# Performance work log

Measured on AMD Instinct MI355X. Metric: run time of the kernel, lower is better.

Reference implementation:

```python
import jax, jax.numpy as jnp
import numpy as np

THRESH = 0.7  # TWN-style threshold factor: delta = 0.7 * mean|W|


def ternarize(W):
    """Quantize latent float weights to alpha * {-1, 0, +1} (per-tensor scale)."""
    absW = jnp.abs(W)
    delta = THRESH * jnp.mean(absW)
    mask = (absW > delta).astype(W.dtype)
    n = jnp.maximum(jnp.sum(mask), 1.0)
    alpha = jnp.sum(absW * mask) / n
    return alpha * jnp.sign(W) * mask


def setup_inputs() -> dict:
    key = jax.random.key(0)
    k_x, k_w1, k_b1, k_w2, k_b2 = jax.random.split(key, 5)
    B = 65536
    x = jax.random.normal(k_x, (B, 784), dtype=jnp.float32)
    # latent float weights (torch Linear layout: [out, in]), kaiming-ish scale
    W1 = jax.random.normal(k_w1, (64, 784), dtype=jnp.float32) * (1.0 / np.sqrt(784))
    b1 = jax.random.normal(k_b1, (64,), dtype=jnp.float32) * 0.01
    W2 = jax.random.normal(k_w2, (10, 64), dtype=jnp.float32) * (1.0 / np.sqrt(64))
    b2 = jax.random.normal(k_b2, (10,), dtype=jnp.float32) * 0.01
    return {"x": x, "W1": W1, "b1": b1, "W2": W2, "b2": b2}


def reference(x, W1, b1, W2, b2):
    x = x.reshape(-1, 784)
    Wq1 = ternarize(W1)  # [64, 784]
    Wq2 = ternarize(W2)  # [10, 64]
    h = jax.nn.relu(x @ Wq1.T + b1)   # [B, 64]
    out = h @ Wq2.T + b2              # [B, 10]
    return out
```

## Files before the change

### kernel.cpp

```cpp
#include <hip/hip_runtime.h>
#include <hip/hip_bf16.h>


typedef __attribute__((ext_vector_type(4))) float f32x4;
typedef __attribute__((ext_vector_type(8))) short s16x8;
typedef __attribute__((ext_vector_type(4))) short s16x4;

#define K1 784
#define K1_PAD 800
#define NHID 64
#define NOUT 10

static __device__ __forceinline__ unsigned short f2bf_rne(float f) {
    unsigned int u = __builtin_bit_cast(unsigned int, f);
    unsigned int r = u + 0x7FFFu + ((u >> 16) & 1u);
    return (unsigned short)(r >> 16);
}

static __device__ double block_sum256(double v, double* red) {
    #pragma unroll
    for (int off = 32; off > 0; off >>= 1) v += __shfl_down(v, off, 64);
    const int w = threadIdx.x >> 6;
    const int lane = threadIdx.x & 63;
    __syncthreads();
    if (lane == 0) red[w] = v;
    __syncthreads();
    return red[0] + red[1] + red[2] + red[3];
}

__global__ __launch_bounds__(256) void tern_sum_kernel(
    const float* __restrict__ W1, const float* __restrict__ W2,
    double* __restrict__ hdr)
{
    __shared__ double red[4];
    double s = 0.0;
    for (int i = blockIdx.x * 256 + threadIdx.x; i < NHID * K1; i += gridDim.x * 256)
        s += (double)fabsf(W1[i]);
    s = block_sum256(s, red);
    if (threadIdx.x == 0) atomicAdd(&hdr[0], s);

    if (blockIdx.x == 0) {
        double s2 = 0.0;
        for (int i = threadIdx.x; i < NOUT * NHID; i += 256)
            s2 += (double)fabsf(W2[i]);
        s2 = block_sum256(s2, red);
        if (threadIdx.x == 0) atomicAdd(&hdr[1], s2);
    }
}

__global__ __launch_bounds__(256) void tern_quant_kernel(
    const float* __restrict__ W1, const float* __restrict__ W2,
    unsigned short* __restrict__ W1q, unsigned short* __restrict__ W2q,
    double* __restrict__ hdr)
{
    __shared__ double red[4];
    const float delta1 = (float)(0.7 * hdr[0] / (double)(NHID * K1));

    double sm = 0.0, cn = 0.0;
    for (int i = blockIdx.x * 256 + threadIdx.x; i < NHID * K1_PAD; i += gridDim.x * 256) {
        int n = i / K1_PAD;
        int k = i - n * K1_PAD;
        unsigned short v = 0;
        if (k < K1) {
            float w = W1[n * K1 + k];
            float a = fabsf(w);
            if (a > delta1) { v = (w > 0.0f) ? 0x3F80u : 0xBF80u; sm += (double)a; cn += 1.0; }
        }
        W1q[i] = v;
    }
    sm = block_sum256(sm, red);
    cn = block_sum256(cn, red);
    if (threadIdx.x == 0) { atomicAdd(&hdr[2], sm); atomicAdd(&hdr[3], cn); }

    if (blockIdx.x == 0) {
        const float delta2 = (float)(0.7 * hdr[1] / (double)(NOUT * NHID));
        double sm2 = 0.0, cn2 = 0.0;
        for (int i = threadIdx.x; i < 16 * NHID; i += 256) {
            int n = i >> 6;
            int k = i & 63;
            unsigned short v = 0;
            if (n < NOUT) {
                float w = W2[n * NHID + k];
                float a = fabsf(w);
                if (a > delta2) { v = (w > 0.0f) ? 0x3F80u : 0xBF80u; sm2 += (double)a; cn2 += 1.0; }
            }
            W2q[i] = v;
        }
        sm2 = block_sum256(sm2, red);
        cn2 = block_sum256(cn2, red);
        if (threadIdx.x == 0) { atomicAdd(&hdr[4], sm2); atomicAdd(&hdr[5], cn2); }
    }
}

__global__ __launch_bounds__(256) void fused_kernel(
    const float* __restrict__ x,
    const float* __restrict__ b1,
    const float* __restrict__ b2,
    const short* __restrict__ W1q,
    const short* __restrict__ W2q,
    const double* __restrict__ hdr,
    float* __restrict__ out)
{
    const int tid  = threadIdx.x;
    const int wave = tid >> 6;
    const int lane = tid & 63;
    const int low  = lane & 15;
    const int quad = lane >> 4;

    const int m0 = blockIdx.x * 64 + wave * 16;

    const int srow = lane >> 3;
    const int scol = lane & 7;
    const float* g0 = x + (size_t)(m0 + srow) * K1 + scol * 4;
    const float* g1 = x + (size_t)(m0 + 8 + srow) * K1 + scol * 4;

    __shared__ __align__(16) unsigned short stage[4][2][16][32];
    __shared__ __align__(16) unsigned short h_lds[4][16][72];

    const short* wbase = W1q + (size_t)low * K1_PAD + quad * 8;

    f32x4 acc[4];
    #pragma unroll
    for (int nt = 0; nt < 4; ++nt) acc[nt] = (f32x4){0.f, 0.f, 0.f, 0.f};

    const f32x4 zero4 = (f32x4){0.f, 0.f, 0.f, 0.f};

    f32x4 c0 = *(const f32x4*)(g0);
    f32x4 c1 = *(const f32x4*)(g1);

    int buf = 0;
    for (int ks = 0; ks < 25; ++ks) {
        f32x4 n0 = zero4, n1 = zero4;
        if (ks < 24) {
            const int kf = (ks + 1) * 32 + scol * 4;
            if (kf < K1) {
                n0 = *(const f32x4*)(g0 + (ks + 1) * 32);
                n1 = *(const f32x4*)(g1 + (ks + 1) * 32);
            }
        }

        s16x4 p0, p1;
        p0[0] = (short)f2bf_rne(c0[0]); p0[1] = (short)f2bf_rne(c0[1]);
        p0[2] = (short)f2bf_rne(c0[2]); p0[3] = (short)f2bf_rne(c0[3]);
        p1[0] = (short)f2bf_rne(c1[0]); p1[1] = (short)f2bf_rne(c1[1]);
        p1[2] = (short)f2bf_rne(c1[2]); p1[3] = (short)f2bf_rne(c1[3]);
        *(s16x4*)&stage[wave][buf][srow][scol * 4]     = p0;
        *(s16x4*)&stage[wave][buf][8 + srow][scol * 4] = p1;

        __asm__ volatile("s_waitcnt lgkmcnt(0)" ::: "memory");

        s16x8 a = *(const s16x8*)&stage[wave][buf][low][quad * 8];
        const short* wk = wbase + ks * 32;
        #pragma unroll
        for (int nt = 0; nt < 4; ++nt) {
            s16x8 b = *(const s16x8*)(wk + (size_t)nt * 16 * K1_PAD);
            acc[nt] = __builtin_amdgcn_mfma_f32_16x16x32_bf16(a, b, acc[nt], 0, 0, 0);
        }

        c0 = n0; c1 = n1; buf ^= 1;
    }

    const float alpha1 = (float)(hdr[2] / fmax(hdr[3], 1.0));
    const float alpha2 = (float)(hdr[4] / fmax(hdr[5], 1.0));

    #pragma unroll
    for (int nt = 0; nt < 4; ++nt) {
        const int n = nt * 16 + low;
        const float bias = b1[n];
        #pragma unroll
        for (int r = 0; r < 4; ++r) {
            float hv = fmaxf(0.0f, fmaf(alpha1, acc[nt][r], bias));
            h_lds[wave][quad * 4 + r][n] = f2bf_rne(hv);
        }
    }
    __asm__ volatile("s_waitcnt lgkmcnt(0)" ::: "memory");

    s16x8 a0 = *(const s16x8*)(&h_lds[wave][low][quad * 8]);
    s16x8 a1 = *(const s16x8*)(&h_lds[wave][low][32 + quad * 8]);
    s16x8 w0 = *(const s16x8*)(W2q + low * 64 + quad * 8);
    s16x8 w1 = *(const s16x8*)(W2q + low * 64 + 32 + quad * 8);

    f32x4 acc2 = (f32x4){0.f, 0.f, 0.f, 0.f};
    acc2 = __builtin_amdgcn_mfma_f32_16x16x32_bf16(a0, w0, acc2, 0, 0, 0);
    acc2 = __builtin_amdgcn_mfma_f32_16x16x32_bf16(a1, w1, acc2, 0, 0, 0);

    if (low < NOUT) {
        const float bias2 = b2[low];
        #pragma unroll
        for (int r = 0; r < 4; ++r) {
            const int row = m0 + quad * 4 + r;
            out[(size_t)row * NOUT + low] = fmaf(alpha2, acc2[r], bias2);
        }
    }
}

extern "C" void kernel_launch(void* const* d_in, const int* in_sizes, int n_in,
                              void* d_out, int out_size, void* d_ws, size_t ws_size,
                              hipStream_t stream) {
    const float* x  = (const float*)d_in[0];
    const float* W1 = (const float*)d_in[1];
    const float* b1 = (const float*)d_in[2];
    const float* W2 = (const float*)d_in[3];
    const float* b2 = (const float*)d_in[4];
    float* out = (float*)d_out;

    const int nrows = in_sizes[0] / K1;

    double* hdr = (double*)d_ws;
    unsigned short* W1q = (unsigned short*)((char*)d_ws + 64);
    unsigned short* W2q = W1q + NHID * K1_PAD;

    hipMemsetAsync(d_ws, 0, 64, stream);

    tern_sum_kernel<<<64, 256, 0, stream>>>(W1, W2, hdr);
    tern_quant_kernel<<<64, 256, 0, stream>>>(W1, W2, W1q, W2q, hdr);

    const int nblocks = nrows / 64;
    fused_kernel<<<nblocks, 256, 0, stream>>>(x, b1, b2, (const short*)W1q,
                                              (const short*)W2q, hdr, out);
}
```

Baseline: 307.6 us.

## Merge ternarization kernels and deepen x prefetch to three stages

```diff
diff --git a/kernel.cpp b/kernel.cpp
--- a/kernel.cpp
+++ b/kernel.cpp
@@ -28,59 +28,45 @@
     return red[0] + red[1] + red[2] + red[3];
 }
 
-__global__ __launch_bounds__(256) void tern_sum_kernel(
+__global__ __launch_bounds__(256) void tern_kernel(
     const float* __restrict__ W1, const float* __restrict__ W2,
-    double* __restrict__ hdr)
+    unsigned short* __restrict__ W1q, unsigned short* __restrict__ W2q,
+    double* __restrict__ parts)
 {
     __shared__ double red[4];
+    const int tid = threadIdx.x;
+
     double s = 0.0;
-    for (int i = blockIdx.x * 256 + threadIdx.x; i < NHID * K1; i += gridDim.x * 256)
-        s += (double)fabsf(W1[i]);
+    for (int i = tid; i < NHID * K1; i += 256) s += (double)fabsf(W1[i]);
     s = block_sum256(s, red);
-    if (threadIdx.x == 0) atomicAdd(&hdr[0], s);
-
-    if (blockIdx.x == 0) {
-        double s2 = 0.0;
-        for (int i = threadIdx.x; i < NOUT * NHID; i += 256)
-            s2 += (double)fabsf(W2[i]);
-        s2 = block_sum256(s2, red);
-        if (threadIdx.x == 0) atomicAdd(&hdr[1], s2);
-    }
-}
-
-__global__ __launch_bounds__(256) void tern_quant_kernel(
-    const float* __restrict__ W1, const float* __restrict__ W2,
-    unsigned short* __restrict__ W1q, unsigned short* __restrict__ W2q,
-    double* __restrict__ hdr)
-{
-    __shared__ double red[4];
-    const float delta1 = (float)(0.7 * hdr[0] / (double)(NHID * K1));
-
+    const float delta1 = (float)(0.7 * (s / (double)(NHID * K1)));
+
+    const int n = blockIdx.x;
     double sm = 0.0, cn = 0.0;
-    for (int i = blockIdx.x * 256 + threadIdx.x; i < NHID * K1_PAD; i += gridDim.x * 256) {
-        int n = i / K1_PAD;
-        int k = i - n * K1_PAD;
+    for (int k = tid; k < K1_PAD; k += 256) {
         unsigned short v = 0;
         if (k < K1) {
             float w = W1[n * K1 + k];
             float a = fabsf(w);
             if (a > delta1) { v = (w > 0.0f) ? 0x3F80u : 0xBF80u; sm += (double)a; cn += 1.0; }
         }
-        W1q[i] = v;
+        W1q[n * K1_PAD + k] = v;
     }
     sm = block_sum256(sm, red);
     cn = block_sum256(cn, red);
-    if (threadIdx.x == 0) { atomicAdd(&hdr[2], sm); atomicAdd(&hdr[3], cn); }
+    if (tid == 0) { parts[n] = sm; parts[64 + n] = cn; }
 
     if (blockIdx.x == 0) {
-        const float delta2 = (float)(0.7 * hdr[1] / (double)(NOUT * NHID));
+        double s2 = 0.0;
+        for (int i = tid; i < NOUT * NHID; i += 256) s2 += (double)fabsf(W2[i]);
+        s2 = block_sum256(s2, red);
+        const float delta2 = (float)(0.7 * (s2 / (double)(NOUT * NHID)));
         double sm2 = 0.0, cn2 = 0.0;
-        for (int i = threadIdx.x; i < 16 * NHID; i += 256) {
-            int n = i >> 6;
-            int k = i & 63;
+        for (int i = tid; i < 16 * NHID; i += 256) {
+            int r = i >> 6, k = i & 63;
             unsigned short v = 0;
-            if (n < NOUT) {
-                float w = W2[n * NHID + k];
+            if (r < NOUT) {
+                float w = W2[r * NHID + k];
                 float a = fabsf(w);
                 if (a > delta2) { v = (w > 0.0f) ? 0x3F80u : 0xBF80u; sm2 += (double)a; cn2 += 1.0; }
             }
@@ -88,7 +74,7 @@
         }
         sm2 = block_sum256(sm2, red);
         cn2 = block_sum256(cn2, red);
-        if (threadIdx.x == 0) { atomicAdd(&hdr[4], sm2); atomicAdd(&hdr[5], cn2); }
+        if (tid == 0) parts[128] = sm2 / fmax(cn2, 1.0);
     }
 }
 
@@ -98,7 +84,7 @@
     const float* __restrict__ b2,
     const short* __restrict__ W1q,
     const short* __restrict__ W2q,
-    const double* __restrict__ hdr,
+    const double* __restrict__ parts,
     float* __restrict__ out)
 {
     const int tid  = threadIdx.x;
@@ -106,37 +92,44 @@
     const int lane = tid & 63;
     const int low  = lane & 15;
     const int quad = lane >> 4;
-
     const int m0 = blockIdx.x * 64 + wave * 16;
 
     const int srow = lane >> 3;
     const int scol = lane & 7;
     const float* g0 = x + (size_t)(m0 + srow) * K1 + scol * 4;
-    const float* g1 = x + (size_t)(m0 + 8 + srow) * K1 + scol * 4;
+    const float* g1 = g0 + 8 * K1;
+    const float* g0t = x + (size_t)(m0 + srow) * K1 + 768 + (scol & 3) * 4;
+    const float* g1t = g0t + 8 * K1;
+
+    const short* wb0 = W1q + (size_t)(low     ) * K1_PAD + quad * 8;
+    const short* wb1 = W1q + (size_t)(low + 16) * K1_PAD + quad * 8;
+    const short* wb2 = W1q + (size_t)(low + 32) * K1_PAD + quad * 8;
+    const short* wb3 = W1q + (size_t)(low + 48) * K1_PAD + quad * 8;
 
     __shared__ __align__(16) unsigned short stage[4][2][16][32];
     __shared__ __align__(16) unsigned short h_lds[4][16][72];
 
-    const short* wbase = W1q + (size_t)low * K1_PAD + quad * 8;
-
     f32x4 acc[4];
     #pragma unroll
     for (int nt = 0; nt < 4; ++nt) acc[nt] = (f32x4){0.f, 0.f, 0.f, 0.f};
 
-    const f32x4 zero4 = (f32x4){0.f, 0.f, 0.f, 0.f};
-
-    f32x4 c0 = *(const f32x4*)(g0);
-    f32x4 c1 = *(const f32x4*)(g1);
-
-    int buf = 0;
+    f32x4 q0[3], q1[3];
+    q0[0] = *(const f32x4*)(g0);       q1[0] = *(const f32x4*)(g1);
+    q0[1] = *(const f32x4*)(g0 + 32);  q1[1] = *(const f32x4*)(g1 + 32);
+    q0[2] = *(const f32x4*)(g0 + 64);  q1[2] = *(const f32x4*)(g1 + 64);
+
+    #pragma unroll
     for (int ks = 0; ks < 25; ++ks) {
-        f32x4 n0 = zero4, n1 = zero4;
-        if (ks < 24) {
-            const int kf = (ks + 1) * 32 + scol * 4;
-            if (kf < K1) {
-                n0 = *(const f32x4*)(g0 + (ks + 1) * 32);
-                n1 = *(const f32x4*)(g1 + (ks + 1) * 32);
-            }
+        const int slot = ks % 3;
+        const int buf  = ks & 1;
+        f32x4 c0 = q0[slot], c1 = q1[slot];
+
+        if (ks + 3 < 24) {
+            q0[slot] = *(const f32x4*)(g0 + (ks + 3) * 32);
+            q1[slot] = *(const f32x4*)(g1 + (ks + 3) * 32);
+        } else if (ks + 3 == 24) {
+            q0[slot] = *(const f32x4*)(g0t);
+            q1[slot] = *(const f32x4*)(g1t);
         }
 
         s16x4 p0, p1;
@@ -150,18 +143,27 @@
         __asm__ volatile("s_waitcnt lgkmcnt(0)" ::: "memory");
 
         s16x8 a = *(const s16x8*)&stage[wave][buf][low][quad * 8];
-        const short* wk = wbase + ks * 32;
-        #pragma unroll
-        for (int nt = 0; nt < 4; ++nt) {
-            s16x8 b = *(const s16x8*)(wk + (size_t)nt * 16 * K1_PAD);
-            acc[nt] = __builtin_amdgcn_mfma_f32_16x16x32_bf16(a, b, acc[nt], 0, 0, 0);
-        }
-
-        c0 = n0; c1 = n1; buf ^= 1;
-    }
-
-    const float alpha1 = (float)(hdr[2] / fmax(hdr[3], 1.0));
-    const float alpha2 = (float)(hdr[4] / fmax(hdr[5], 1.0));
+        s16x8 bf0 = *(const s16x8*)(wb0 + ks * 32);
+        s16x8 bf1 = *(const s16x8*)(wb1 + ks * 32);
+        s16x8 bf2 = *(const s16x8*)(wb2 + ks * 32);
+        s16x8 bf3 = *(const s16x8*)(wb3 + ks * 32);
+        acc[0] = __builtin_amdgcn_mfma_f32_16x16x32_bf16(a, bf0, acc[0], 0, 0, 0);
+        acc[1] = __builtin_amdgcn_mfma_f32_16x16x32_bf16(a, bf1, acc[1], 0, 0, 0);
+        acc[2] = __builtin_amdgcn_mfma_f32_16x16x32_bf16(a, bf2, acc[2], 0, 0, 0);
+        acc[3] = __builtin_amdgcn_mfma_f32_16x16x32_bf16(a, bf3, acc[3], 0, 0, 0);
+    }
+
+    double smd = parts[lane];
+    double cnd = parts[64 + lane];
+    #pragma unroll
+    for (int off = 32; off > 0; off >>= 1) {
+        smd += __shfl_down(smd, off, 64);
+        cnd += __shfl_down(cnd, off, 64);
+    }
+    smd = __shfl(smd, 0, 64);
+    cnd = __shfl(cnd, 0, 64);
+    const float alpha1 = (float)(smd / fmax(cnd, 1.0));
+    const float alpha2 = (float)parts[128];
 
     #pragma unroll
     for (int nt = 0; nt < 4; ++nt) {
@@ -206,16 +208,13 @@
 
     const int nrows = in_sizes[0] / K1;
 
-    double* hdr = (double*)d_ws;
-    unsigned short* W1q = (unsigned short*)((char*)d_ws + 64);
+    double* parts = (double*)d_ws;
+    unsigned short* W1q = (unsigned short*)((char*)d_ws + 2048);
     unsigned short* W2q = W1q + NHID * K1_PAD;
 
-    hipMemsetAsync(d_ws, 0, 64, stream);
-
-    tern_sum_kernel<<<64, 256, 0, stream>>>(W1, W2, hdr);
-    tern_quant_kernel<<<64, 256, 0, stream>>>(W1, W2, W1q, W2q, hdr);
+    tern_kernel<<<64, 256, 0, stream>>>(W1, W2, W1q, W2q, parts);
 
     const int nblocks = nrows / 64;
     fused_kernel<<<nblocks, 256, 0, stream>>>(x, b1, b2, (const short*)W1q,
-                                              (const short*)W2q, hdr, out);
-}
+                                              (const short*)W2q, parts, out);
+}
```

New measurement: 378.8 us. 1.23x slower.
